# Performance work log

Measured on AMD Instinct MI355X. Metric: run time of the kernel, lower is better.

The kernel has to match this reference:

```python
import jax, jax.numpy as jnp
import numpy as np

N_STMT, N_FUNC = 100000, 50000
T, V, C, H, L, E = 16, 50000, 128, 8, 2, 200000
D = C // H  # per-head dim = 16
N_NODES = (N_STMT, N_FUNC)
# (src_type, dst_type) for the 3 relations: stmt->stmt, stmt->func, func->stmt
EDGE_TYPES = ((0, 0), (0, 1), (1, 0))


def _segment_softmax(logits, seg, num_segments):
    # logits: [E, H], seg: [E] destination node ids
    m = jax.ops.segment_max(logits, seg, num_segments)
    m = jnp.where(jnp.isfinite(m), m, 0.0)
    e = jnp.exp(logits - m[seg])
    s = jax.ops.segment_sum(e, seg, num_segments)
    return e / (s[seg] + 1e-16)


def setup_inputs() -> dict:
    key = jax.random.key(0)
    ks = jax.random.split(key, 24)
    nrm = lambda k, sh, s=0.1: jax.random.normal(k, sh, dtype=jnp.float32) * s
    ri = lambda k, sh, hi: jax.random.randint(k, sh, 0, hi, dtype=jnp.int32)
    return {
        "tok_stmt": ri(ks[0], (N_STMT, T), V),
        "tok_func": ri(ks[1], (N_FUNC, T), V),
        "e0_src": ri(ks[2], (E,), N_STMT), "e0_dst": ri(ks[3], (E,), N_STMT),
        "e1_src": ri(ks[4], (E,), N_STMT), "e1_dst": ri(ks[5], (E,), N_FUNC),
        "e2_src": ri(ks[6], (E,), N_FUNC), "e2_dst": ri(ks[7], (E,), N_STMT),
        "emb": nrm(ks[8], (V, C), 0.5),
        "lin_w": nrm(ks[9], (2, C, C)), "lin_b": jnp.zeros((2, C), jnp.float32),
        "kw": nrm(ks[10], (L, 2, C, C)), "kb": jnp.zeros((L, 2, C), jnp.float32),
        "qw": nrm(ks[11], (L, 2, C, C)), "qb": jnp.zeros((L, 2, C), jnp.float32),
        "vw": nrm(ks[12], (L, 2, C, C)), "vb": jnp.zeros((L, 2, C), jnp.float32),
        "aw": nrm(ks[13], (L, 2, C, C)), "ab": jnp.zeros((L, 2, C), jnp.float32),
        "skip": jnp.ones((L, 2), jnp.float32),
        "a_rel": nrm(ks[14], (L, 3, H, D, D), 0.25),
        "m_rel": nrm(ks[15], (L, 3, H, D, D), 0.25),
        "p_rel": jnp.ones((L, 3, H), jnp.float32),
    }


def _hgt_forward(tok_stmt, tok_func, edges, emb, lin_w, lin_b,
                 kw, kb, qw, qb, vw, vb, aw, ab, skip, a_rel, m_rel, p_rel):
    # STEncoder (embedding + mean pool) + relu, then per-type linear + relu
    xs = []
    for t, tok in enumerate((tok_stmt, tok_func)):
        e = jax.nn.relu(jnp.mean(emb[tok], axis=1))          # [N_t, C]
        xs.append(jax.nn.relu(e @ lin_w[t] + lin_b[t]))      # [N_t, C]

    scale = 1.0 / jnp.sqrt(jnp.float32(D))
    for l in range(L):
        k = [(x @ kw[l, t] + kb[l, t]).reshape(-1, H, D) for t, x in enumerate(xs)]
        q = [(x @ qw[l, t] + qb[l, t]).reshape(-1, H, D) for t, x in enumerate(xs)]
        v = [(x @ vw[l, t] + vb[l, t]).reshape(-1, H, D) for t, x in enumerate(xs)]
        agg = [jnp.zeros((N_NODES[t], H, D), xs[t].dtype) for t in range(2)]
        for r, (st, dt) in enumerate(EDGE_TYPES):
            src, dst = edges[r]
            k_r = jnp.einsum('nhd,hde->nhe', k[st], a_rel[l, r])
            v_r = jnp.einsum('nhd,hde->nhe', v[st], m_rel[l, r])
            logits = jnp.sum(q[dt][dst] * k_r[src], axis=-1) * p_rel[l, r] * scale  # [E,H]
            alpha = _segment_softmax(logits, dst, N_NODES[dt])
            msg = v_r[src] * alpha[..., None]                 # [E,H,D]
            agg[dt] = agg[dt] + jax.ops.segment_sum(msg, dst, N_NODES[dt])
        new_xs = []
        for t in range(2):
            o = jax.nn.gelu(agg[t].reshape(N_NODES[t], C))
            o = o @ aw[l, t] + ab[l, t]
            g = jax.nn.sigmoid(skip[l, t])
            new_xs.append(g * o + (1.0 - g) * xs[t])
        xs = new_xs
    return jnp.concatenate(xs, axis=0)  # [N_STMT + N_FUNC, C]


def reference(tok_stmt, tok_func, e0_src, e0_dst, e1_src, e1_dst, e2_src, e2_dst,
              emb, lin_w, lin_b, kw, kb, qw, qb, vw, vb, aw, ab, skip,
              a_rel, m_rel, p_rel):
    edges = ((e0_src, e0_dst), (e1_src, e1_dst), (e2_src, e2_dst))
    return _hgt_forward(tok_stmt, tok_func, edges, emb, lin_w, lin_b,
                        kw, kb, qw, qb, vw, vb, aw, ab, skip, a_rel, m_rel, p_rel)
```

## Files before the change

### kernel.cpp

```cpp
#include <hip/hip_runtime.h>
#include <hip/hip_bf16.h>


typedef __hip_bfloat16 bf16;
typedef __attribute__((ext_vector_type(8))) short short8;
typedef __attribute__((ext_vector_type(4))) short s4v;
typedef __attribute__((ext_vector_type(4))) float floatx4;

#define N_STMT 100000
#define N_FUNC 50000
#define N_TOT  150000
#define EDGES  200000
#define CCH 128
#define RPB2 96
#define GS2 1042
#define GF2 521
#define GA 782
#define GB 1042
#define GF 391
#define EB 782

__device__ __forceinline__ float b2f(bf16 x){ return __bfloat162float(x); }
__device__ __forceinline__ float bs2f(short s){
  union { short s; bf16 h; } u; u.s = s; return __bfloat162float(u.h);
}
__device__ __forceinline__ short f2bs(float x){
  union { bf16 h; short s; } u; u.h = __float2bfloat16(x); return u.s;
}
__device__ __forceinline__ float blo(unsigned u){ return __uint_as_float(u << 16); }
__device__ __forceinline__ float bhi(unsigned u){ return __uint_as_float(u & 0xffff0000u); }
__device__ __forceinline__ float gelu_f(float x){
  float z = 1.5957691216057308f * (x + 0.044715f * x * x * x);
  float t = __expf(z);
  return x - x / (t + 1.f);
}

__global__ __launch_bounds__(256) void prep_all(
    const float* __restrict__ emb, bf16* __restrict__ ebf,
    const float* __restrict__ lin_w, const float* __restrict__ qw,
    const float* __restrict__ aw, bf16* __restrict__ WT,
    const float* __restrict__ kw, const float* __restrict__ kb,
    const float* __restrict__ vw, const float* __restrict__ vb,
    const float* __restrict__ a_rel, const float* __restrict__ m_rel,
    bf16* __restrict__ WRT, float* __restrict__ Bf)
{
  int bid = blockIdx.x;
  if (bid < 3125) {
    long i = ((long)bid * 256 + threadIdx.x) * 8;
    float4 f0 = *(const float4*)(emb + i);
    float4 f1 = *(const float4*)(emb + i + 4);
    short8 o;
    o[0]=f2bs(f0.x); o[1]=f2bs(f0.y); o[2]=f2bs(f0.z); o[3]=f2bs(f0.w);
    o[4]=f2bs(f1.x); o[5]=f2bs(f1.y); o[6]=f2bs(f1.z); o[7]=f2bs(f1.w);
    *(short8*)(ebf + i) = o;
  } else if (bid < 3765) {
    int lb = bid - 3125;
    int mat = lb >> 6;
    const float* src = (mat < 2) ? lin_w + mat * 16384
                     : (mat < 6) ? qw + (mat - 2) * 16384
                                 : aw + (mat - 6) * 16384;
    bf16* dst = WT + mat * 16384;
    int idx = (lb & 63) * 256 + threadIdx.x;
    int n = idx >> 7, k = idx & 127;
    dst[idx] = __float2bfloat16(src[k * 128 + n]);
  } else {
    int lb = bid - 3765;
    int y = lb >> 6;
    bool isV = y >= 6;
    int z = isV ? y - 6 : y;
    int l = z / 3, r = z % 3, st = (r == 2) ? 1 : 0;
    const float* W   = (isV ? vw : kw) + (l * 2 + st) * 16384;
    const float* b   = (isV ? vb : kb) + (l * 2 + st) * 128;
    const float* rel = (isV ? m_rel : a_rel) + z * 2048;
    bf16* Wrt = WRT + y * 16384;
    float* br = Bf + y * 128;

    int idx = (lb & 63) * 256 + threadIdx.x;
    if (idx < 128 * 128) {
      int c = idx >> 7, o = idx & 127;
      int h = o >> 4, e = o & 15;
      float acc = 0.f;
#pragma unroll
      for (int d = 0; d < 16; d++)
        acc += W[c * 128 + h * 16 + d] * rel[h * 256 + d * 16 + e];
      Wrt[o * 128 + c] = __float2bfloat16(acc);
    }
    if (idx < 128) {
      int h = idx >> 4, e = idx & 15;
      float acc = 0.f;
#pragma unroll
      for (int d = 0; d < 16; d++)
        acc += b[h * 16 + d] * rel[h * 256 + d * 16 + e];
      br[idx] = acc;
    }
  }
}

__global__ __launch_bounds__(256) void pool_embed(
    const int* __restrict__ tok_s, const int* __restrict__ tok_f,
    const bf16* __restrict__ ebf, bf16* __restrict__ E_out)
{
  int n = blockIdx.x * 4 + (threadIdx.x >> 6);
  int lane = threadIdx.x & 63, g = lane >> 4, c16 = lane & 15;
  const int* tok = (n < N_STMT) ? (tok_s + n * 16) : (tok_f + (n - N_STMT) * 16);
  float acc[8] = {0.f,0.f,0.f,0.f,0.f,0.f,0.f,0.f};
#pragma unroll
  for (int j = 0; j < 4; j++) {
    int v = tok[g * 4 + j];
    short8 row = *(const short8*)(ebf + (long)v * CCH + c16 * 8);
#pragma unroll
    for (int q = 0; q < 8; q++) acc[q] += bs2f(row[q]);
  }
#pragma unroll
  for (int q = 0; q < 8; q++) {
    acc[q] += __shfl_xor(acc[q], 16);
    acc[q] += __shfl_xor(acc[q], 32);
  }
  if (g == 0) {
    short8 o;
#pragma unroll
    for (int q = 0; q < 8; q++) o[q] = f2bs(fmaxf(acc[q] * (1.f/16.f), 0.f));
    *(short8*)(E_out + (long)n * CCH + c16 * 8) = o;
  }
}

template <bool RELU, bool BLEND, bool OUT_BF16>
__global__ __launch_bounds__(256) void gemm_2t_reg(
    const bf16* __restrict__ Ab, const bf16* __restrict__ Wt0,
    const bf16* __restrict__ Wt1, const float* __restrict__ bias0,
    const float* __restrict__ bias1, const bf16* __restrict__ oldx,
    void* __restrict__ dstv, const float* __restrict__ skip2)
{
  const int wave = threadIdx.x >> 6, lane = threadIdx.x & 63;
  const int lane15 = lane & 15, quad = lane >> 4;
  const int jc0 = wave * 2;
  const int bid = blockIdx.x;
  const int type = (bid >= GS2);
  const long base = type ? (long)N_STMT * CCH : 0;
  const int Nrows = type ? N_FUNC : N_STMT;
  long row = (long)(type ? bid - GS2 : bid) * RPB2;
  long rowEnd = row + RPB2; if (rowEnd > Nrows) rowEnd = Nrows;
  const bf16* Wt = type ? Wt1 : Wt0;
  const float* bias = type ? bias1 : bias0;

  short8 w[2][4];
#pragma unroll
  for (int jj = 0; jj < 2; jj++)
#pragma unroll
    for (int kq = 0; kq < 4; kq++)
      w[jj][kq] = *(const short8*)(
          Wt + ((jc0 + jj) * 16 + lane15) * CCH + kq * 32 + quad * 8);
  float4 bb[2];
#pragma unroll
  for (int jj = 0; jj < 2; jj++)
    bb[jj] = *(const float4*)(bias + (jc0 + jj) * 16 + quad * 4);

  float g = 1.f, gi = 0.f;
  if (BLEND) {
    float sk = skip2[type];
    g = 1.f / (1.f + expf(-sk));
    gi = 1.f - g;
  }

  short8 a[4];
  {
    long r = row + lane15; if (r >= Nrows) r = Nrows - 1;
#pragma unroll
    for (int kq = 0; kq < 4; kq++)
      a[kq] = *(const short8*)(Ab + base + r * CCH + kq * 32 + quad * 8);
  }

  for (; row < rowEnd; row += 16) {
    short8 an[4];
    {
      long nrow = (row + 16 < rowEnd) ? row + 16 : row;
      long r = nrow + lane15; if (r >= Nrows) r = Nrows - 1;
#pragma unroll
      for (int kq = 0; kq < 4; kq++)
        an[kq] = *(const short8*)(Ab + base + r * CCH + kq * 32 + quad * 8);
    }

    floatx4 acc[2];
#pragma unroll
    for (int jj = 0; jj < 2; jj++) {
      acc[jj][0] = bb[jj].x; acc[jj][1] = bb[jj].y;
      acc[jj][2] = bb[jj].z; acc[jj][3] = bb[jj].w;
    }
#pragma unroll
    for (int kq = 0; kq < 4; kq++)
#pragma unroll
      for (int jj = 0; jj < 2; jj++)
        acc[jj] = __builtin_amdgcn_mfma_f32_16x16x32_bf16(
            w[jj][kq], a[kq], acc[jj], 0, 0, 0);

    long r = row + lane15;
    if (r < Nrows) {
#pragma unroll
      for (int jj = 0; jj < 2; jj++) {
        int c0 = (jc0 + jj) * 16 + quad * 4;
        long idx = base + r * CCH + c0;
        float v[4];
#pragma unroll
        for (int q = 0; q < 4; q++) v[q] = acc[jj][q];
        if (RELU) {
#pragma unroll
          for (int q = 0; q < 4; q++) v[q] = fmaxf(v[q], 0.f);
        }
        if (BLEND) {
          s4v ov = *(const s4v*)(oldx + idx);
#pragma unroll
          for (int q = 0; q < 4; q++) v[q] = g * v[q] + gi * bs2f(ov[q]);
        }
        if (OUT_BF16) {
          s4v o;
#pragma unroll
          for (int q = 0; q < 4; q++) o[q] = f2bs(v[q]);
          *(s4v*)((bf16*)dstv + idx) = o;
        } else {
          float4 o = make_float4(v[0], v[1], v[2], v[3]);
          *(float4*)((float*)dstv + idx) = o;
        }
      }
    }
#pragma unroll
    for (int kq = 0; kq < 4; kq++) a[kq] = an[kq];
  }
}

template <int NM, bool HASQ>
__device__ __forceinline__ void qkv_body(
    const bf16* __restrict__ Ab,
    const bf16* __restrict__ W0, const float* __restrict__ B0,
    const bf16* __restrict__ W1, const float* __restrict__ B1,
    const bf16* __restrict__ W2, const float* __restrict__ B2,
    bf16* __restrict__ Q, bf16* __restrict__ KV, int N, int rpb, int bid)
{
  const int wave = threadIdx.x >> 6, lane = threadIdx.x & 63;
  const int lane15 = lane & 15, quad = lane >> 4;
  const int jc0 = wave * 2;
  constexpr int KIDX = HASQ ? 1 : 0;
  constexpr int VIDX = KIDX + 1;

  long row = (long)bid * rpb;
  if (row >= N) return;
  long rowEnd = row + rpb; if (rowEnd > N) rowEnd = N;

  const bf16* Wm[3]  = {W0, W1, W2};
  const float* Bm[3] = {B0, B1, B2};

  short8 w[NM][2][4];
#pragma unroll
  for (int m = 0; m < NM; m++)
#pragma unroll
    for (int jj = 0; jj < 2; jj++)
#pragma unroll
      for (int kq = 0; kq < 4; kq++)
        w[m][jj][kq] = *(const short8*)(
            Wm[m] + ((jc0 + jj) * 16 + lane15) * CCH + kq * 32 + quad * 8);

  for (; row < rowEnd; row += 16) {
    long r = row + lane15;
    long rc = (r < N) ? r : (N - 1);
    short8 a[4];
#pragma unroll
    for (int kq = 0; kq < 4; kq++)
      a[kq] = *(const short8*)(Ab + rc * CCH + kq * 32 + quad * 8);

    floatx4 acc[NM][2];
#pragma unroll
    for (int m = 0; m < NM; m++)
#pragma unroll
      for (int jj = 0; jj < 2; jj++) {
        float4 bb = *(const float4*)(Bm[m] + (jc0 + jj) * 16 + quad * 4);
        acc[m][jj][0] = bb.x; acc[m][jj][1] = bb.y;
        acc[m][jj][2] = bb.z; acc[m][jj][3] = bb.w;
      }

#pragma unroll
    for (int kq = 0; kq < 4; kq++)
#pragma unroll
      for (int m = 0; m < NM; m++)
#pragma unroll
        for (int jj = 0; jj < 2; jj++)
          acc[m][jj] = __builtin_amdgcn_mfma_f32_16x16x32_bf16(
              w[m][jj][kq], a[kq], acc[m][jj], 0, 0, 0);

    if (r < N) {
#pragma unroll
      for (int jj = 0; jj < 2; jj++) {
        int c0 = (jc0 + jj) * 16 + quad * 4;
        if constexpr (HASQ) {
          s4v qo;
          qo[0] = f2bs(acc[0][jj][0]);
          qo[1] = f2bs(acc[0][jj][1]);
          qo[2] = f2bs(acc[0][jj][2]);
          qo[3] = f2bs(acc[0][jj][3]);
          *(s4v*)(Q + r * CCH + c0) = qo;
        }
        short8 kv;
        kv[0] = f2bs(acc[KIDX][jj][0]);
        kv[1] = f2bs(acc[KIDX][jj][1]);
        kv[2] = f2bs(acc[VIDX][jj][0]);
        kv[3] = f2bs(acc[VIDX][jj][1]);
        kv[4] = f2bs(acc[KIDX][jj][2]);
        kv[5] = f2bs(acc[KIDX][jj][3]);
        kv[6] = f2bs(acc[VIDX][jj][2]);
        kv[7] = f2bs(acc[VIDX][jj][3]);
        *(short8*)(KV + r * 256 + 2 * c0) = kv;
      }
    }
  }
}

__global__ __launch_bounds__(256, 3) void qkv_all(
    const bf16* __restrict__ Xb, const bf16* __restrict__ WT,
    const bf16* __restrict__ WRT, const float* __restrict__ Bf,
    const float* __restrict__ qb,
    bf16* __restrict__ Qb, bf16* __restrict__ KV0,
    bf16* __restrict__ KV1, bf16* __restrict__ KV2, int l)
{
  const int bid = blockIdx.x;
  const int z0 = l * 3 + 0, z1 = l * 3 + 1, z2 = l * 3 + 2;
  if (bid < GA) {
    qkv_body<3, true>(Xb,
        WT + (2 + l * 2) * 16384, qb + (l * 2) * 128,
        WRT + z0 * 16384, Bf + z0 * 128,
        WRT + (6 + z0) * 16384, Bf + (6 + z0) * 128,
        Qb, KV0, N_STMT, 128, bid);
  } else if (bid < GA + GB) {
    qkv_body<2, false>(Xb,
        WRT + z1 * 16384, Bf + z1 * 128,
        WRT + (6 + z1) * 16384, Bf + (6 + z1) * 128,
        nullptr, nullptr,
        nullptr, KV1, N_STMT, 96, bid - GA);
  } else {
    qkv_body<3, true>(Xb + (long)N_STMT * CCH,
        WT + (2 + l * 2 + 1) * 16384, qb + (l * 2 + 1) * 128,
        WRT + z2 * 16384, Bf + z2 * 128,
        WRT + (6 + z2) * 16384, Bf + (6 + z2) * 128,
        Qb + (long)N_STMT * CCH, KV2, N_FUNC, 128, bid - GA - GB);
  }
}

__global__ __launch_bounds__(256) void csr_count_all(
    const int* __restrict__ d0, const int* __restrict__ d1,
    const int* __restrict__ d2, int* __restrict__ degf,
    int* __restrict__ posf)
{
  int r = blockIdx.x / EB;
  int e = (blockIdx.x % EB) * 256 + threadIdx.x;
  if (e < EDGES) {
    const int* dst = r == 0 ? d0 : r == 1 ? d1 : d2;
    int off = r == 0 ? 0 : r == 1 ? 100000 : 150000;
    posf[r * EDGES + e] = atomicAdd(&degf[off + dst[e]], 1);
  }
}
__global__ __launch_bounds__(256) void csr_alloc_all(
    const int* __restrict__ degf, int* __restrict__ rowstartf,
    int* __restrict__ total)
{
  int bid = blockIdx.x;
  int r, base, Nd, lb;
  if (bid < 391)      { r = 0; base = 0;      Nd = 100000; lb = bid; }
  else if (bid < 587) { r = 1; base = 100000; Nd = 50000;  lb = bid - 391; }
  else                { r = 2; base = 150000; Nd = 100000; lb = bid - 587; }
  int n = lb * 256 + threadIdx.x;
  if (n < Nd) rowstartf[base + n] = atomicAdd(total + r, degf[base + n]);
}
__global__ __launch_bounds__(256) void csr_fill_all(
    const int* __restrict__ d0, const int* __restrict__ d1,
    const int* __restrict__ d2, const int* __restrict__ s0,
    const int* __restrict__ s1, const int* __restrict__ s2,
    const int* __restrict__ rowstartf, const int* __restrict__ posf,
    int* __restrict__ srcs0, int* __restrict__ srcs1, int* __restrict__ srcs2)
{
  int r = blockIdx.x / EB;
  int e = (blockIdx.x % EB) * 256 + threadIdx.x;
  if (e < EDGES) {
    const int* dst = r == 0 ? d0 : r == 1 ? d1 : d2;
    const int* src = r == 0 ? s0 : r == 1 ? s1 : s2;
    int* sr = r == 0 ? srcs0 : r == 1 ? srcs1 : srcs2;
    int off = r == 0 ? 0 : r == 1 ? 100000 : 150000;
    sr[rowstartf[off + dst[e]] + posf[r * EDGES + e]] = src[e];
  }
}

__device__ __forceinline__ void relmsg_grp(
    int rs, int g, const int* __restrict__ srcs,
    const bf16* __restrict__ KV, float psc,
    const float* __restrict__ q, int lane, float* __restrict__ out)
{
  int p = lane & 15;
  int gbase = lane & 48;
  float den = 0.f;
  float a[8] = {0.f,0.f,0.f,0.f,0.f,0.f,0.f,0.f};
  for (int j0 = 0; j0 < g; j0 += 16) {
    int rem = g - j0; if (rem > 16) rem = 16;
    int sl = srcs[rs + j0 + (p < rem ? p : rem - 1)];
    for (int j = 0; j < rem; j++) {
      int s = __shfl(sl, gbase + j);
      const bf16* rowp = KV + (long)s * 256 + 16 * p;
      uint4 u0 = *(const uint4*)(rowp);
      uint4 u1 = *(const uint4*)(rowp + 8);
      float prod = q[0]*blo(u0.x) + q[1]*bhi(u0.x)
                 + q[2]*blo(u0.z) + q[3]*bhi(u0.z)
                 + q[4]*blo(u1.x) + q[5]*bhi(u1.x)
                 + q[6]*blo(u1.z) + q[7]*bhi(u1.z);
      prod += __shfl_xor(prod, 1);
      float ev = __expf(prod * psc);
      den += ev;
      a[0] += ev * blo(u0.y); a[1] += ev * bhi(u0.y);
      a[2] += ev * blo(u0.w); a[3] += ev * bhi(u0.w);
      a[4] += ev * blo(u1.y); a[5] += ev * bhi(u1.y);
      a[6] += ev * blo(u1.w); a[7] += ev * bhi(u1.w);
    }
  }
  float inv = 1.f / (den + 1e-16f);
#pragma unroll
  for (int i = 0; i < 8; i++) out[i] = a[i] * inv;
}

__global__ __launch_bounds__(256) void agg_all(
    const int* __restrict__ rs0, const int* __restrict__ dg0, const int* __restrict__ srcs0,
    const int* __restrict__ rs1, const int* __restrict__ dg1, const int* __restrict__ srcs1,
    const int* __restrict__ rs2, const int* __restrict__ dg2, const int* __restrict__ srcs2,
    const bf16* __restrict__ KV0, const bf16* __restrict__ KV1,
    const bf16* __restrict__ KV2, const float* __restrict__ pl,
    const bf16* __restrict__ Qb, bf16* __restrict__ AGGb)
{
  int n = blockIdx.x * 16 + (threadIdx.x >> 4);
  if (n >= N_TOT) return;
  int lane = threadIdx.x & 63;
  int p = lane & 15, h = p >> 1;
  uint4 qv = *(const uint4*)(Qb + (long)n * CCH + 8 * p);
  float q[8];
  q[0] = blo(qv.x); q[1] = bhi(qv.x); q[2] = blo(qv.y); q[3] = bhi(qv.y);
  q[4] = blo(qv.z); q[5] = bhi(qv.z); q[6] = blo(qv.w); q[7] = bhi(qv.w);
  float m[8];
  if (n < N_STMT) {
    float m0[8], m2[8];
    relmsg_grp(rs0[n], dg0[n], srcs0, KV0, pl[h] * 0.25f, q, lane, m0);
    relmsg_grp(rs2[n], dg2[n], srcs2, KV2, pl[16 + h] * 0.25f, q, lane, m2);
#pragma unroll
    for (int i = 0; i < 8; i++) m[i] = m0[i] + m2[i];
  } else {
    int nf = n - N_STMT;
    relmsg_grp(rs1[nf], dg1[nf], srcs1, KV1, pl[8 + h] * 0.25f, q, lane, m);
  }
  short8 o;
#pragma unroll
  for (int i = 0; i < 8; i++) o[i] = f2bs(gelu_f(m[i]));
  *(short8*)(AGGb + (long)n * CCH + 8 * p) = o;
}

__global__ __launch_bounds__(256) void zero_out_k(float* __restrict__ out)
{
  long i = ((long)blockIdx.x * 256 + threadIdx.x) * 4;
  *(float4*)(out + i) = make_float4(0.f, 0.f, 0.f, 0.f);
}

extern "C" void kernel_launch(void* const* d_in, const int* in_sizes, int n_in,
                              void* d_out, int out_size, void* d_ws, size_t ws_size,
                              hipStream_t stream)
{
  const int* tok_s = (const int*)d_in[0];
  const int* tok_f = (const int*)d_in[1];
  const int* esrc[3] = {(const int*)d_in[2], (const int*)d_in[4], (const int*)d_in[6]};
  const int* edst[3] = {(const int*)d_in[3], (const int*)d_in[5], (const int*)d_in[7]};
  const float* emb   = (const float*)d_in[8];
  const float* lin_w = (const float*)d_in[9];
  const float* lin_b = (const float*)d_in[10];
  const float* kw = (const float*)d_in[11];
  const float* kb = (const float*)d_in[12];
  const float* qw = (const float*)d_in[13];
  const float* qb = (const float*)d_in[14];
  const float* vw = (const float*)d_in[15];
  const float* vb = (const float*)d_in[16];
  const float* aw = (const float*)d_in[17];
  const float* ab = (const float*)d_in[18];
  const float* skip  = (const float*)d_in[19];
  const float* a_rel = (const float*)d_in[20];
  const float* m_rel = (const float*)d_in[21];
  const float* p_rel = (const float*)d_in[22];

  float* Bf   = (float*)d_ws;
  bf16*  Xb   = (bf16*)(Bf + 1536);
  bf16*  AGGb = Xb  + 19200000L;
  bf16*  KV0  = AGGb + 19200000L;
  bf16*  KV1  = KV0 + 25600000L;
  bf16*  KV2  = KV1 + 25600000L;
  bf16*  WT   = KV2 + 12800000L;
  bf16*  WRT  = WT  + 163840L;
  int*   ip   = (int*)(WRT + 196608L);
  int* degf        = ip;
  int* total       = ip + 250000;
  int* rowstartf   = ip + 250004;
  int* rowstart[3] = {ip + 250004, ip + 350004, ip + 400004};
  int* deg[3]      = {ip, ip + 100000, ip + 150000};
  int* srcs[3]     = {ip + 500004, ip + 700004, ip + 900004};
  int* posf        = ip + 1100004;
  bf16* EBF   = KV0;
  bf16*  Qb   = (bf16*)d_out;
  float* OUTF = (float*)d_out;

  const size_t NEED = (size_t)1536 * 4 + (size_t)102760448 * 2
                    + (size_t)1700004 * 4;
  if (ws_size < NEED) {
    zero_out_k<<<19200000 / 4 / 256, 256, 0, stream>>>(OUTF);
    return;
  }

  hipMemsetAsync(ip, 0, (size_t)250004 * 4, stream);
  csr_count_all<<<3 * EB, 256, 0, stream>>>(
      edst[0], edst[1], edst[2], degf, posf);
  csr_alloc_all<<<978, 256, 0, stream>>>(degf, rowstartf, total);
  csr_fill_all<<<3 * EB, 256, 0, stream>>>(
      edst[0], edst[1], edst[2], esrc[0], esrc[1], esrc[2],
      rowstartf, posf, srcs[0], srcs[1], srcs[2]);

  prep_all<<<4533, 256, 0, stream>>>(
      emb, EBF, lin_w, qw, aw, WT, kw, kb, vw, vb, a_rel, m_rel, WRT, Bf);

  pool_embed<<<N_TOT / 4, 256, 0, stream>>>(tok_s, tok_f, EBF, AGGb);
  gemm_2t_reg<true, false, true><<<GS2 + GF2, 256, 0, stream>>>(
      AGGb, WT, WT + 16384, lin_b, lin_b + 128, nullptr, Xb, nullptr);

  for (int l = 0; l < 2; l++) {
    qkv_all<<<GA + GB + GF, 256, 0, stream>>>(
        Xb, WT, WRT, Bf, qb, Qb, KV0, KV1, KV2, l);
    agg_all<<<(N_TOT + 15) / 16, 256, 0, stream>>>(
        rowstart[0], deg[0], srcs[0], rowstart[1], deg[1], srcs[1],
        rowstart[2], deg[2], srcs[2], KV0, KV1, KV2,
        p_rel + l * 24, Qb, AGGb);
    if (l == 0)
      gemm_2t_reg<false, true, true><<<GS2 + GF2, 256, 0, stream>>>(
          AGGb, WT + 6 * 16384, WT + 7 * 16384, ab, ab + 128,
          Xb, Xb, skip);
    else
      gemm_2t_reg<false, true, false><<<GS2 + GF2, 256, 0, stream>>>(
          AGGb, WT + 8 * 16384, WT + 9 * 16384, ab + 256, ab + 384,
          Xb, OUTF, skip + 2);
  }
}
```

Measured before the change: 679.2 us.

## Merge CSR build kernels into front-end prep, pool and GEMM launches

```diff
diff --git a/kernel.cpp b/kernel.cpp
--- a/kernel.cpp
+++ b/kernel.cpp
@@ -19,6 +19,8 @@
 #define GB 1042
 #define GF 391
 #define EB 782
+#define PREPB 4533
+#define POOLB 37500
 
 __device__ __forceinline__ float b2f(bf16 x){ return __bfloat162float(x); }
 __device__ __forceinline__ float bs2f(short s){
@@ -35,8 +37,9 @@
   return x - x / (t + 1.f);
 }
 
-__global__ __launch_bounds__(256) void prep_all(
-    const float* __restrict__ emb, bf16* __restrict__ ebf,
+
+__device__ __forceinline__ void prep_body(
+    int bid, const float* __restrict__ emb, bf16* __restrict__ ebf,
     const float* __restrict__ lin_w, const float* __restrict__ qw,
     const float* __restrict__ aw, bf16* __restrict__ WT,
     const float* __restrict__ kw, const float* __restrict__ kb,
@@ -44,7 +47,6 @@
     const float* __restrict__ a_rel, const float* __restrict__ m_rel,
     bf16* __restrict__ WRT, float* __restrict__ Bf)
 {
-  int bid = blockIdx.x;
   if (bid < 3125) {
     long i = ((long)bid * 256 + threadIdx.x) * 8;
     float4 f0 = *(const float4*)(emb + i);
@@ -96,11 +98,11 @@
   }
 }
 
-__global__ __launch_bounds__(256) void pool_embed(
-    const int* __restrict__ tok_s, const int* __restrict__ tok_f,
+__device__ __forceinline__ void pool_body(
+    int bid, const int* __restrict__ tok_s, const int* __restrict__ tok_f,
     const bf16* __restrict__ ebf, bf16* __restrict__ E_out)
 {
-  int n = blockIdx.x * 4 + (threadIdx.x >> 6);
+  int n = bid * 4 + (threadIdx.x >> 6);
   int lane = threadIdx.x & 63, g = lane >> 4, c16 = lane & 15;
   const int* tok = (n < N_STMT) ? (tok_s + n * 16) : (tok_f + (n - N_STMT) * 16);
   float acc[8] = {0.f,0.f,0.f,0.f,0.f,0.f,0.f,0.f};
@@ -125,8 +127,8 @@
 }
 
 template <bool RELU, bool BLEND, bool OUT_BF16>
-__global__ __launch_bounds__(256) void gemm_2t_reg(
-    const bf16* __restrict__ Ab, const bf16* __restrict__ Wt0,
+__device__ __forceinline__ void gemm_2t_body(
+    int bid, const bf16* __restrict__ Ab, const bf16* __restrict__ Wt0,
     const bf16* __restrict__ Wt1, const float* __restrict__ bias0,
     const float* __restrict__ bias1, const bf16* __restrict__ oldx,
     void* __restrict__ dstv, const float* __restrict__ skip2)
@@ -134,7 +136,6 @@
   const int wave = threadIdx.x >> 6, lane = threadIdx.x & 63;
   const int lane15 = lane & 15, quad = lane >> 4;
   const int jc0 = wave * 2;
-  const int bid = blockIdx.x;
   const int type = (bid >= GS2);
   const long base = type ? (long)N_STMT * CCH : 0;
   const int Nrows = type ? N_FUNC : N_STMT;
@@ -225,6 +226,95 @@
 #pragma unroll
     for (int kq = 0; kq < 4; kq++) a[kq] = an[kq];
   }
+}
+
+
+__global__ __launch_bounds__(256) void front1(
+    const float* __restrict__ emb, bf16* __restrict__ ebf,
+    const float* __restrict__ lin_w, const float* __restrict__ qw,
+    const float* __restrict__ aw, bf16* __restrict__ WT,
+    const float* __restrict__ kw, const float* __restrict__ kb,
+    const float* __restrict__ vw, const float* __restrict__ vb,
+    const float* __restrict__ a_rel, const float* __restrict__ m_rel,
+    bf16* __restrict__ WRT, float* __restrict__ Bf,
+    const int* __restrict__ d0, const int* __restrict__ d1,
+    const int* __restrict__ d2, int* __restrict__ degf,
+    int* __restrict__ posf)
+{
+  int bid = blockIdx.x;
+  if (bid < PREPB) {
+    prep_body(bid, emb, ebf, lin_w, qw, aw, WT, kw, kb, vw, vb,
+              a_rel, m_rel, WRT, Bf);
+  } else {
+    int lb = bid - PREPB;
+    int r = lb / EB;
+    int e = (lb % EB) * 256 + threadIdx.x;
+    if (e < EDGES) {
+      const int* dst = r == 0 ? d0 : r == 1 ? d1 : d2;
+      int off = r == 0 ? 0 : r == 1 ? 100000 : 150000;
+      posf[r * EDGES + e] = atomicAdd(&degf[off + dst[e]], 1);
+    }
+  }
+}
+
+__global__ __launch_bounds__(256) void front2(
+    const int* __restrict__ tok_s, const int* __restrict__ tok_f,
+    const bf16* __restrict__ ebf, bf16* __restrict__ E_out,
+    const int* __restrict__ degf, int* __restrict__ rowstartf,
+    int* __restrict__ total)
+{
+  int bid = blockIdx.x;
+  if (bid < POOLB) {
+    pool_body(bid, tok_s, tok_f, ebf, E_out);
+  } else {
+    int lb = bid - POOLB;
+    int r, base, Nd, b2;
+    if (lb < 391)      { r = 0; base = 0;      Nd = 100000; b2 = lb; }
+    else if (lb < 587) { r = 1; base = 100000; Nd = 50000;  b2 = lb - 391; }
+    else               { r = 2; base = 150000; Nd = 100000; b2 = lb - 587; }
+    int n = b2 * 256 + threadIdx.x;
+    if (n < Nd) rowstartf[base + n] = atomicAdd(total + r, degf[base + n]);
+  }
+}
+
+__global__ __launch_bounds__(256) void front3(
+    const bf16* __restrict__ Ab, const bf16* __restrict__ Wt0,
+    const bf16* __restrict__ Wt1, const float* __restrict__ bias0,
+    const float* __restrict__ bias1, bf16* __restrict__ Xb,
+    const int* __restrict__ d0, const int* __restrict__ d1,
+    const int* __restrict__ d2, const int* __restrict__ s0,
+    const int* __restrict__ s1, const int* __restrict__ s2,
+    const int* __restrict__ rowstartf, const int* __restrict__ posf,
+    int* __restrict__ srcs0, int* __restrict__ srcs1, int* __restrict__ srcs2)
+{
+  int bid = blockIdx.x;
+  if (bid < GS2 + GF2) {
+    gemm_2t_body<true, false, true>(bid, Ab, Wt0, Wt1, bias0, bias1,
+                                    nullptr, Xb, nullptr);
+  } else {
+    int lb = bid - (GS2 + GF2);
+    int r = lb / EB;
+    int e = (lb % EB) * 256 + threadIdx.x;
+    if (e < EDGES) {
+      const int* dst = r == 0 ? d0 : r == 1 ? d1 : d2;
+      const int* src = r == 0 ? s0 : r == 1 ? s1 : s2;
+      int* sr = r == 0 ? srcs0 : r == 1 ? srcs1 : srcs2;
+      int off = r == 0 ? 0 : r == 1 ? 100000 : 150000;
+      sr[rowstartf[off + dst[e]] + posf[r * EDGES + e]] = src[e];
+    }
+  }
+}
+
+
+template <bool RELU, bool BLEND, bool OUT_BF16>
+__global__ __launch_bounds__(256) void gemm_2t_reg(
+    const bf16* __restrict__ Ab, const bf16* __restrict__ Wt0,
+    const bf16* __restrict__ Wt1, const float* __restrict__ bias0,
+    const float* __restrict__ bias1, const bf16* __restrict__ oldx,
+    void* __restrict__ dstv, const float* __restrict__ skip2)
+{
+  gemm_2t_body<RELU, BLEND, OUT_BF16>(blockIdx.x, Ab, Wt0, Wt1, bias0, bias1,
+                                      oldx, dstv, skip2);
 }
 
 template <int NM, bool HASQ>
@@ -339,49 +429,6 @@
         WRT + z2 * 16384, Bf + z2 * 128,
         WRT + (6 + z2) * 16384, Bf + (6 + z2) * 128,
         Qb + (long)N_STMT * CCH, KV2, N_FUNC, 128, bid - GA - GB);
-  }
-}
-
-__global__ __launch_bounds__(256) void csr_count_all(
-    const int* __restrict__ d0, const int* __restrict__ d1,
-    const int* __restrict__ d2, int* __restrict__ degf,
-    int* __restrict__ posf)
-{
-  int r = blockIdx.x / EB;
-  int e = (blockIdx.x % EB) * 256 + threadIdx.x;
-  if (e < EDGES) {
-    const int* dst = r == 0 ? d0 : r == 1 ? d1 : d2;
-    int off = r == 0 ? 0 : r == 1 ? 100000 : 150000;
-    posf[r * EDGES + e] = atomicAdd(&degf[off + dst[e]], 1);
-  }
-}
-__global__ __launch_bounds__(256) void csr_alloc_all(
-    const int* __restrict__ degf, int* __restrict__ rowstartf,
-    int* __restrict__ total)
-{
-  int bid = blockIdx.x;
-  int r, base, Nd, lb;
-  if (bid < 391)      { r = 0; base = 0;      Nd = 100000; lb = bid; }
-  else if (bid < 587) { r = 1; base = 100000; Nd = 50000;  lb = bid - 391; }
-  else                { r = 2; base = 150000; Nd = 100000; lb = bid - 587; }
-  int n = lb * 256 + threadIdx.x;
-  if (n < Nd) rowstartf[base + n] = atomicAdd(total + r, degf[base + n]);
-}
-__global__ __launch_bounds__(256) void csr_fill_all(
-    const int* __restrict__ d0, const int* __restrict__ d1,
-    const int* __restrict__ d2, const int* __restrict__ s0,
-    const int* __restrict__ s1, const int* __restrict__ s2,
-    const int* __restrict__ rowstartf, const int* __restrict__ posf,
-    int* __restrict__ srcs0, int* __restrict__ srcs1, int* __restrict__ srcs2)
-{
-  int r = blockIdx.x / EB;
-  int e = (blockIdx.x % EB) * 256 + threadIdx.x;
-  if (e < EDGES) {
-    const int* dst = r == 0 ? d0 : r == 1 ? d1 : d2;
-    const int* src = r == 0 ? s0 : r == 1 ? s1 : s2;
-    int* sr = r == 0 ? srcs0 : r == 1 ? srcs1 : srcs2;
-    int off = r == 0 ? 0 : r == 1 ? 100000 : 150000;
-    sr[rowstartf[off + dst[e]] + posf[r * EDGES + e]] = src[e];
   }
 }
 
@@ -511,19 +558,15 @@
   }
 
   hipMemsetAsync(ip, 0, (size_t)250004 * 4, stream);
-  csr_count_all<<<3 * EB, 256, 0, stream>>>(
+  front1<<<PREPB + 3 * EB, 256, 0, stream>>>(
+      emb, EBF, lin_w, qw, aw, WT, kw, kb, vw, vb, a_rel, m_rel, WRT, Bf,
       edst[0], edst[1], edst[2], degf, posf);
-  csr_alloc_all<<<978, 256, 0, stream>>>(degf, rowstartf, total);
-  csr_fill_all<<<3 * EB, 256, 0, stream>>>(
+  front2<<<POOLB + 978, 256, 0, stream>>>(
+      tok_s, tok_f, EBF, AGGb, degf, rowstartf, total);
+  front3<<<GS2 + GF2 + 3 * EB, 256, 0, stream>>>(
+      AGGb, WT, WT + 16384, lin_b, lin_b + 128, Xb,
       edst[0], edst[1], edst[2], esrc[0], esrc[1], esrc[2],
       rowstartf, posf, srcs[0], srcs[1], srcs[2]);
-
-  prep_all<<<4533, 256, 0, stream>>>(
-      emb, EBF, lin_w, qw, aw, WT, kw, kb, vw, vb, a_rel, m_rel, WRT, Bf);
-
-  pool_embed<<<N_TOT / 4, 256, 0, stream>>>(tok_s, tok_f, EBF, AGGb);
-  gemm_2t_reg<true, false, true><<<GS2 + GF2, 256, 0, stream>>>(
-      AGGb, WT, WT + 16384, lin_b, lin_b + 128, nullptr, Xb, nullptr);
 
   for (int l = 0; l < 2; l++) {
     qkv_all<<<GA + GB + GF, 256, 0, stream>>>(
```

New measurement: 666.1 us. No clear change (-1.9%).
